# Optimization experiments

Measured on AMD Instinct MI355X. Metric: run time of the kernel, lower is better.

Reference implementation:

```python
import jax, jax.numpy as jnp
import numpy as np

N = 50000
E = 800000
IN_C = 128
HID = 64
HEADS = 4
OUT_C = 64
NEG_SLOPE = 0.2


def _glorot(key, shape):
    fan = shape[0] + shape[-1]
    return jax.random.normal(key, shape, dtype=jnp.float32) * jnp.sqrt(2.0 / fan)


def setup_inputs() -> dict:
    key = jax.random.key(0)
    ks = jax.random.split(key, 12)
    x = jax.random.normal(ks[0], (N, IN_C), dtype=jnp.float32)
    edge_index = jax.random.randint(ks[1], (2, E), 0, N, dtype=jnp.int64)
    edge_attr = jax.random.normal(ks[2], (E, 8), dtype=jnp.float32)
    # gat1: in -> heads*hid
    W1 = _glorot(ks[3], (IN_C, HEADS * HID))
    att_src1 = _glorot(ks[4], (HEADS, HID))
    att_dst1 = _glorot(ks[5], (HEADS, HID))
    b1 = jnp.zeros((HEADS * HID,), dtype=jnp.float32)
    # gat2: heads*hid -> out, 1 head
    W2 = _glorot(ks[6], (HEADS * HID, OUT_C))
    att_src2 = _glorot(ks[7], (1, OUT_C))
    att_dst2 = _glorot(ks[8], (1, OUT_C))
    b2 = jnp.zeros((OUT_C,), dtype=jnp.float32)
    return {"x": x, "edge_index": edge_index, "edge_attr": edge_attr,
            "W1": W1, "att_src1": att_src1, "att_dst1": att_dst1, "b1": b1,
            "W2": W2, "att_src2": att_src2, "att_dst2": att_dst2, "b2": b2}


def _gat_conv(x, src, dst, W, att_src, att_dst, b, heads, n_nodes):
    # x: [N, Cin] -> h: [N, H, C]
    h = (x @ W).reshape(n_nodes, heads, -1)
    a_src = jnp.sum(h * att_src, axis=-1)  # [N, H]
    a_dst = jnp.sum(h * att_dst, axis=-1)  # [N, H]
    e = jax.nn.leaky_relu(a_src[src] + a_dst[dst], NEG_SLOPE)  # [Etot, H]
    # segment softmax over destination node (self-loops guarantee non-empty segments)
    m = jax.ops.segment_max(e, dst, num_segments=n_nodes)      # [N, H]
    w = jnp.exp(e - m[dst])
    denom = jax.ops.segment_sum(w, dst, num_segments=n_nodes)  # [N, H]
    alpha = w / (denom[dst] + 1e-16)                           # [Etot, H]
    out = jax.ops.segment_sum(alpha[:, :, None] * h[src], dst, num_segments=n_nodes)
    return out.reshape(n_nodes, -1) + b  # concat heads (identity when heads==1)


def reference(x, edge_index, edge_attr, W1, att_src1, att_dst1, b1, W2, att_src2, att_dst2, b2):
    # PyG GATConv with edge_dim=None ignores edge_attr; add_self_loops=True by default.
    loop = jnp.arange(N, dtype=edge_index.dtype)
    src = jnp.concatenate([edge_index[0], loop])
    dst = jnp.concatenate([edge_index[1], loop])
    h = jax.nn.elu(_gat_conv(x, src, dst, W1, att_src1, att_dst1, b1, HEADS, N))
    out = jax.nn.elu(_gat_conv(h, src, dst, W2, att_src2, att_dst2, b2, 1, N))
    return out
```

## Files before the change

kernel.cpp:

```cpp
#include <hip/hip_runtime.h>
#include <hip/hip_bf16.h>
#include <math.h>

#define LEAKY 0.2f

#define BM 64
#define BN 64
#define BK 32
__global__ __launch_bounds__(256) void gemm_att(const float* __restrict__ A,
                                                const float* __restrict__ B,
                                                float* __restrict__ C,
                                                const float* __restrict__ att_s,
                                                const float* __restrict__ att_d,
                                                float* __restrict__ asrc,
                                                float* __restrict__ adst,
                                                int M, int K, int NC) {
    __shared__ float As[BK][BM + 1];
    __shared__ float Bs[BK][BN];
    const int tid = threadIdx.x;
    const int bm = blockIdx.x * BM;
    const int bn = blockIdx.y * BN;
    const int tx = tid & 15, ty = tid >> 4;
    float acc[4][4] = {};
    for (int k0 = 0; k0 < K; k0 += BK) {
        #pragma unroll
        for (int i = 0; i < (BM * BK) / 256; ++i) {
            int idx = tid + i * 256;
            int r = idx >> 5, c = idx & 31;
            int gr = bm + r;
            As[c][r] = (gr < M) ? A[(size_t)gr * K + k0 + c] : 0.f;
        }
        #pragma unroll
        for (int i = 0; i < (BK * BN) / 256; ++i) {
            int idx = tid + i * 256;
            int r = idx >> 6, c = idx & 63;
            Bs[r][c] = B[(size_t)(k0 + r) * NC + bn + c];
        }
        __syncthreads();
        #pragma unroll
        for (int k = 0; k < BK; ++k) {
            float a[4], b[4];
            #pragma unroll
            for (int i = 0; i < 4; ++i) a[i] = As[k][ty * 4 + i];
            #pragma unroll
            for (int j = 0; j < 4; ++j) b[j] = Bs[k][tx * 4 + j];
            #pragma unroll
            for (int i = 0; i < 4; ++i)
                #pragma unroll
                for (int j = 0; j < 4; ++j)
                    acc[i][j] += a[i] * b[j];
        }
        __syncthreads();
    }
    float s_att[4], d_att[4];
    #pragma unroll
    for (int j = 0; j < 4; ++j) {
        s_att[j] = att_s[bn + tx * 4 + j];
        d_att[j] = att_d[bn + tx * 4 + j];
    }
    const int head = bn >> 6;
    const int H = NC >> 6;
    #pragma unroll
    for (int i = 0; i < 4; ++i) {
        int gr = bm + ty * 4 + i;
        float ps = 0.f, pd = 0.f;
        #pragma unroll
        for (int j = 0; j < 4; ++j) {
            ps += acc[i][j] * s_att[j];
            pd += acc[i][j] * d_att[j];
        }
        #pragma unroll
        for (int o = 1; o < 16; o <<= 1) {
            ps += __shfl_xor(ps, o);
            pd += __shfl_xor(pd, o);
        }
        if (gr < M) {
            #pragma unroll
            for (int j = 0; j < 4; ++j)
                C[(size_t)gr * NC + bn + tx * 4 + j] = acc[i][j];
            if (tx == 0) {
                asrc[gr * H + head] = ps;
                adst[gr * H + head] = pd;
            }
        }
    }
}

__global__ __launch_bounds__(256) void count_deg(const int* __restrict__ ei, int E_, int N_,
                                                 int* __restrict__ deg) {
    int eid = blockIdx.x * 256 + threadIdx.x;
    int Etot = E_ + N_;
    if (eid >= Etot) return;
    int dst = (eid < E_) ? ei[E_ + eid] : (eid - E_);
    atomicAdd(&deg[dst], 1);
}

__global__ __launch_bounds__(1024) void scan_offsets(const int* __restrict__ deg,
                                                     int* __restrict__ off, int n) {
    __shared__ int wsum[16];
    int tid = threadIdx.x;
    int lane = tid & 63, w = tid >> 6;
    int chunk = (n + 1023) / 1024;
    int b = tid * chunk;
    int e = min(b + chunk, n);
    int s = 0;
    for (int i = b; i < e; ++i) s += deg[i];
    int v = s;
    #pragma unroll
    for (int o = 1; o < 64; o <<= 1) {
        int t = __shfl_up(v, o);
        if (lane >= o) v += t;
    }
    if (lane == 63) wsum[w] = v;
    __syncthreads();
    if (w == 0) {
        int t = (lane < 16) ? wsum[lane] : 0;
        #pragma unroll
        for (int o = 1; o < 16; o <<= 1) {
            int u = __shfl_up(t, o);
            if (lane >= o) t += u;
        }
        if (lane < 16) wsum[lane] = t;
    }
    __syncthreads();
    int acc = (w > 0 ? wsum[w - 1] : 0) + (v - s);
    for (int i = b; i < e; ++i) { off[i] = acc; acc += deg[i]; }
    if (e == n) off[n] = acc;
}

__global__ __launch_bounds__(256) void scatter_edges(const int* __restrict__ ei, int E_, int N_,
                                                     int* __restrict__ off,
                                                     int* __restrict__ csr) {
    int eid = blockIdx.x * 256 + threadIdx.x;
    int Etot = E_ + N_;
    if (eid >= Etot) return;
    int src, dst;
    if (eid < E_) { src = ei[eid]; dst = ei[E_ + eid]; }
    else          { src = dst = eid - E_; }
    int pos = atomicAdd(&off[dst], 1);
    csr[pos] = src;
}

__global__ __launch_bounds__(256) void gat_agg_h4(const int* __restrict__ off,
                                                  const int* __restrict__ csr,
                                                  const float* __restrict__ asrc,
                                                  const float* __restrict__ adst,
                                                  const float* __restrict__ hsrc,
                                                  const float* __restrict__ bias,
                                                  float* __restrict__ outp, int N_) {
    int head = threadIdx.x >> 6;
    int lane = threadIdx.x & 63;
    int node = blockIdx.x;
    if (node >= N_) return;
    int s = node ? off[node - 1] : 0;
    int e = off[node];
    float ad = adst[node * 4 + head];
    float m = -INFINITY;
    for (int i = s + lane; i < e; i += 64) {
        float ev = asrc[csr[i] * 4 + head] + ad;
        ev = ev > 0.f ? ev : LEAKY * ev;
        m = fmaxf(m, ev);
    }
    #pragma unroll
    for (int o = 32; o > 0; o >>= 1) m = fmaxf(m, __shfl_xor(m, o));
    float a = 0.f, d = 0.f;
    for (int i = s; i < e; ++i) {
        int u = csr[i];
        float ev = asrc[u * 4 + head] + ad;
        ev = ev > 0.f ? ev : LEAKY * ev;
        float w = __expf(ev - m);
        d += w;
        a += w * hsrc[(size_t)u * 256 + head * 64 + lane];
    }
    float v = a / (d + 1e-16f) + bias[head * 64 + lane];
    outp[(size_t)node * 256 + head * 64 + lane] = v > 0.f ? v : expm1f(v);
}

__global__ __launch_bounds__(256) void gat_agg_h1(const int* __restrict__ off,
                                                  const int* __restrict__ csr,
                                                  const float* __restrict__ asrc,
                                                  const float* __restrict__ adst,
                                                  const float* __restrict__ g,
                                                  const float* __restrict__ bias,
                                                  float* __restrict__ outp, int N_) {
    int wv = threadIdx.x >> 6, lane = threadIdx.x & 63;
    int node = blockIdx.x * 4 + wv;
    if (node >= N_) return;
    int s = node ? off[node - 1] : 0;
    int e = off[node];
    float ad = adst[node];
    float mm = -INFINITY;
    for (int i = s + lane; i < e; i += 64) {
        float ev = asrc[csr[i]] + ad;
        ev = ev > 0.f ? ev : LEAKY * ev;
        mm = fmaxf(mm, ev);
    }
    #pragma unroll
    for (int o = 32; o > 0; o >>= 1) mm = fmaxf(mm, __shfl_xor(mm, o));
    float a = 0.f, d = 0.f;
    for (int i = s; i < e; ++i) {
        int u = csr[i];
        float ev = asrc[u] + ad;
        ev = ev > 0.f ? ev : LEAKY * ev;
        float w = __expf(ev - mm);
        d += w;
        a += w * g[(size_t)u * 64 + lane];
    }
    float v = a / (d + 1e-16f) + bias[lane];
    outp[(size_t)node * 64 + lane] = v > 0.f ? v : expm1f(v);
}

extern "C" void kernel_launch(void* const* d_in, const int* in_sizes, int n_in,
                              void* d_out, int out_size, void* d_ws, size_t ws_size,
                              hipStream_t stream) {
    const float* x        = (const float*)d_in[0];
    const int*   ei       = (const int*)d_in[1];
    const float* W1       = (const float*)d_in[3];
    const float* att_src1 = (const float*)d_in[4];
    const float* att_dst1 = (const float*)d_in[5];
    const float* b1       = (const float*)d_in[6];
    const float* W2       = (const float*)d_in[7];
    const float* att_src2 = (const float*)d_in[8];
    const float* att_dst2 = (const float*)d_in[9];
    const float* b2       = (const float*)d_in[10];
    float* out = (float*)d_out;

    const int N = in_sizes[0] / 128;
    const int E = in_sizes[1] / 2;
    const int Etot = E + N;

    float* ws    = (float*)d_ws;
    float* h1    = ws;
    float* h2    = h1 + (size_t)N * 256;
    float* g2    = h1;
    float* asrc1 = h2 + (size_t)N * 256;
    float* adst1 = asrc1 + (size_t)N * 4;
    float* asrc2 = adst1 + (size_t)N * 4;
    float* adst2 = asrc2 + N;
    int*   deg   = (int*)(adst2 + N);
    int*   off   = deg + (N + 1);
    int*   csr   = off + (N + 1);

    hipMemsetAsync(deg, 0, (N + 1) * sizeof(int), stream);
    count_deg<<<(Etot + 255) / 256, 256, 0, stream>>>(ei, E, N, deg);
    scan_offsets<<<1, 1024, 0, stream>>>(deg, off, N);
    scatter_edges<<<(Etot + 255) / 256, 256, 0, stream>>>(ei, E, N, off, csr);

    {
        dim3 g((N + BM - 1) / BM, 256 / BN);
        gemm_att<<<g, 256, 0, stream>>>(x, W1, h1, att_src1, att_dst1, asrc1, adst1, N, 128, 256);
    }
    gat_agg_h4<<<N, 256, 0, stream>>>(off, csr, asrc1, adst1, h1, b1, h2, N);

    {
        dim3 g((N + BM - 1) / BM, 64 / BN);
        gemm_att<<<g, 256, 0, stream>>>(h2, W2, g2, att_src2, att_dst2, asrc2, adst2, N, 256, 64);
    }
    gat_agg_h1<<<(N + 3) / 4, 256, 0, stream>>>(off, csr, asrc2, adst2, g2, b2, out, N);
}
```

Measured before the change: 705.6 us.

## Remap 4-head aggregation to one wavefront per node and unroll edge loops

The four-head aggregation kernel now assigns one 64-lane wavefront per node, with each lane handling all four heads. Attention scores are loaded as float4 and each lane accumulates four heads in registers. This removes the duplicated per-head csr/asrc traversal and the max pass done by four separate wavefronts per node. Both aggregation kernels also unroll the edge loop (by 2 and by 4) so several independent gathers are in flight at once, at the cost of more registers per thread.

```diff
diff --git a/kernel.cpp b/kernel.cpp
--- a/kernel.cpp
+++ b/kernel.cpp
@@ -148,32 +148,66 @@
                                                   const float* __restrict__ hsrc,
                                                   const float* __restrict__ bias,
                                                   float* __restrict__ outp, int N_) {
-    int head = threadIdx.x >> 6;
-    int lane = threadIdx.x & 63;
-    int node = blockIdx.x;
+    int wv = threadIdx.x >> 6, lane = threadIdx.x & 63;
+    int node = blockIdx.x * 4 + wv;
     if (node >= N_) return;
     int s = node ? off[node - 1] : 0;
     int e = off[node];
-    float ad = adst[node * 4 + head];
-    float m = -INFINITY;
+    float4 ad = *(const float4*)(adst + node * 4);
+    float m0 = -INFINITY, m1 = -INFINITY, m2 = -INFINITY, m3 = -INFINITY;
     for (int i = s + lane; i < e; i += 64) {
-        float ev = asrc[csr[i] * 4 + head] + ad;
-        ev = ev > 0.f ? ev : LEAKY * ev;
-        m = fmaxf(m, ev);
-    }
-    #pragma unroll
-    for (int o = 32; o > 0; o >>= 1) m = fmaxf(m, __shfl_xor(m, o));
-    float a = 0.f, d = 0.f;
-    for (int i = s; i < e; ++i) {
         int u = csr[i];
-        float ev = asrc[u * 4 + head] + ad;
-        ev = ev > 0.f ? ev : LEAKY * ev;
-        float w = __expf(ev - m);
-        d += w;
-        a += w * hsrc[(size_t)u * 256 + head * 64 + lane];
-    }
-    float v = a / (d + 1e-16f) + bias[head * 64 + lane];
-    outp[(size_t)node * 256 + head * 64 + lane] = v > 0.f ? v : expm1f(v);
+        float4 as = *(const float4*)(asrc + u * 4);
+        float e0 = as.x + ad.x; e0 = e0 > 0.f ? e0 : LEAKY * e0; m0 = fmaxf(m0, e0);
+        float e1 = as.y + ad.y; e1 = e1 > 0.f ? e1 : LEAKY * e1; m1 = fmaxf(m1, e1);
+        float e2 = as.z + ad.z; e2 = e2 > 0.f ? e2 : LEAKY * e2; m2 = fmaxf(m2, e2);
+        float e3 = as.w + ad.w; e3 = e3 > 0.f ? e3 : LEAKY * e3; m3 = fmaxf(m3, e3);
+    }
+    #pragma unroll
+    for (int o = 32; o > 0; o >>= 1) {
+        m0 = fmaxf(m0, __shfl_xor(m0, o));
+        m1 = fmaxf(m1, __shfl_xor(m1, o));
+        m2 = fmaxf(m2, __shfl_xor(m2, o));
+        m3 = fmaxf(m3, __shfl_xor(m3, o));
+    }
+    float a0 = 0.f, a1 = 0.f, a2 = 0.f, a3 = 0.f;
+    float d0 = 0.f, d1 = 0.f, d2 = 0.f, d3 = 0.f;
+    int i = s;
+    for (; i + 2 <= e; i += 2) {
+        int u0 = csr[i], u1 = csr[i + 1];
+        float4 as0 = *(const float4*)(asrc + u0 * 4);
+        float4 as1 = *(const float4*)(asrc + u1 * 4);
+        const float* hp0 = hsrc + (size_t)u0 * 256 + lane;
+        const float* hp1 = hsrc + (size_t)u1 * 256 + lane;
+        float g00 = hp0[0], g01 = hp0[64], g02 = hp0[128], g03 = hp0[192];
+        float g10 = hp1[0], g11 = hp1[64], g12 = hp1[128], g13 = hp1[192];
+        float ev, w;
+        ev = as0.x + ad.x; ev = ev > 0.f ? ev : LEAKY * ev; w = __expf(ev - m0); d0 += w; a0 += w * g00;
+        ev = as0.y + ad.y; ev = ev > 0.f ? ev : LEAKY * ev; w = __expf(ev - m1); d1 += w; a1 += w * g01;
+        ev = as0.z + ad.z; ev = ev > 0.f ? ev : LEAKY * ev; w = __expf(ev - m2); d2 += w; a2 += w * g02;
+        ev = as0.w + ad.w; ev = ev > 0.f ? ev : LEAKY * ev; w = __expf(ev - m3); d3 += w; a3 += w * g03;
+        ev = as1.x + ad.x; ev = ev > 0.f ? ev : LEAKY * ev; w = __expf(ev - m0); d0 += w; a0 += w * g10;
+        ev = as1.y + ad.y; ev = ev > 0.f ? ev : LEAKY * ev; w = __expf(ev - m1); d1 += w; a1 += w * g11;
+        ev = as1.z + ad.z; ev = ev > 0.f ? ev : LEAKY * ev; w = __expf(ev - m2); d2 += w; a2 += w * g12;
+        ev = as1.w + ad.w; ev = ev > 0.f ? ev : LEAKY * ev; w = __expf(ev - m3); d3 += w; a3 += w * g13;
+    }
+    if (i < e) {
+        int u = csr[i];
+        float4 as = *(const float4*)(asrc + u * 4);
+        const float* hp = hsrc + (size_t)u * 256 + lane;
+        float g0 = hp[0], g1 = hp[64], g2 = hp[128], g3 = hp[192];
+        float ev, w;
+        ev = as.x + ad.x; ev = ev > 0.f ? ev : LEAKY * ev; w = __expf(ev - m0); d0 += w; a0 += w * g0;
+        ev = as.y + ad.y; ev = ev > 0.f ? ev : LEAKY * ev; w = __expf(ev - m1); d1 += w; a1 += w * g1;
+        ev = as.z + ad.z; ev = ev > 0.f ? ev : LEAKY * ev; w = __expf(ev - m2); d2 += w; a2 += w * g2;
+        ev = as.w + ad.w; ev = ev > 0.f ? ev : LEAKY * ev; w = __expf(ev - m3); d3 += w; a3 += w * g3;
+    }
+    size_t ob = (size_t)node * 256 + lane;
+    float v;
+    v = a0 / (d0 + 1e-16f) + bias[lane];       outp[ob]       = v > 0.f ? v : expm1f(v);
+    v = a1 / (d1 + 1e-16f) + bias[lane + 64];  outp[ob + 64]  = v > 0.f ? v : expm1f(v);
+    v = a2 / (d2 + 1e-16f) + bias[lane + 128]; outp[ob + 128] = v > 0.f ? v : expm1f(v);
+    v = a3 / (d3 + 1e-16f) + bias[lane + 192]; outp[ob + 192] = v > 0.f ? v : expm1f(v);
 }
 
 __global__ __launch_bounds__(256) void gat_agg_h1(const int* __restrict__ off,
@@ -198,7 +232,21 @@
     #pragma unroll
     for (int o = 32; o > 0; o >>= 1) mm = fmaxf(mm, __shfl_xor(mm, o));
     float a = 0.f, d = 0.f;
-    for (int i = s; i < e; ++i) {
+    int i = s;
+    for (; i + 4 <= e; i += 4) {
+        int u0 = csr[i], u1 = csr[i + 1], u2 = csr[i + 2], u3 = csr[i + 3];
+        float s0 = asrc[u0], s1 = asrc[u1], s2 = asrc[u2], s3 = asrc[u3];
+        float g0 = g[(size_t)u0 * 64 + lane];
+        float g1 = g[(size_t)u1 * 64 + lane];
+        float g2 = g[(size_t)u2 * 64 + lane];
+        float g3 = g[(size_t)u3 * 64 + lane];
+        float ev, w;
+        ev = s0 + ad; ev = ev > 0.f ? ev : LEAKY * ev; w = __expf(ev - mm); d += w; a += w * g0;
+        ev = s1 + ad; ev = ev > 0.f ? ev : LEAKY * ev; w = __expf(ev - mm); d += w; a += w * g1;
+        ev = s2 + ad; ev = ev > 0.f ? ev : LEAKY * ev; w = __expf(ev - mm); d += w; a += w * g2;
+        ev = s3 + ad; ev = ev > 0.f ? ev : LEAKY * ev; w = __expf(ev - mm); d += w; a += w * g3;
+    }
+    for (; i < e; ++i) {
         int u = csr[i];
         float ev = asrc[u] + ad;
         ev = ev > 0.f ? ev : LEAKY * ev;
@@ -250,7 +298,7 @@
         dim3 g((N + BM - 1) / BM, 256 / BN);
         gemm_att<<<g, 256, 0, stream>>>(x, W1, h1, att_src1, att_dst1, asrc1, adst1, N, 128, 256);
     }
-    gat_agg_h4<<<N, 256, 0, stream>>>(off, csr, asrc1, adst1, h1, b1, h2, N);
+    gat_agg_h4<<<(N + 3) / 4, 256, 0, stream>>>(off, csr, asrc1, adst1, h1, b1, h2, N);
 
     {
         dim3 g((N + BM - 1) / BM, 64 / BN);
```

After: 581.0 us. 1.21x faster.
